# Kernel tuning notes

Measured on AMD Instinct MI355X. Metric: run time of the kernel, lower is better.

## Reference

```python
import math
import jax, jax.numpy as jnp
import numpy as np

B, T, C = 2, 2048, 2048
H, G = 16, 4
D = C // H  # head_dim = 128
KV = G * D
SOFT_CAP = 50.0
EPS = 1e-6


def setup_inputs() -> dict:
    key = jax.random.key(0)
    ks = jax.random.split(key, 5)
    s = 1.0 / math.sqrt(C)
    return {
        "x": jax.random.normal(ks[0], (B, T, C), jnp.float32),
        "Wq": jax.random.normal(ks[1], (C, C), jnp.float32) * s,
        "Wk": jax.random.normal(ks[2], (KV, C), jnp.float32) * s,
        "Wv": jax.random.normal(ks[3], (KV, C), jnp.float32) * s,
        "Wo": jax.random.normal(ks[4], (C, C), jnp.float32) * s,
        "bo": jnp.zeros((C,), jnp.float32),
        "q_norm_w": jnp.ones((D,), jnp.float32),
        "k_norm_w": jnp.ones((D,), jnp.float32),
    }


def _rmsnorm(x, w):
    # norm/sqrt(d) formulation, eps added to rms (matches torch module exactly)
    rms = jnp.linalg.norm(x, axis=-1, keepdims=True) / math.sqrt(x.shape[-1])
    return w * (x / (rms + EPS))


def _rotary_tables(seq_len, dim):
    inv_freq = 1.0 / (10000.0 ** (jnp.arange(0, dim, 2, dtype=jnp.float32) / dim))
    t = jnp.arange(seq_len, dtype=jnp.float32)
    freqs = jnp.outer(t, inv_freq)  # [T, D/2]
    return jnp.cos(freqs), jnp.sin(freqs)


def _apply_rope(x, cos, sin):
    # x: [B, T, h, D]; cos/sin: [T, D/2] broadcast as [1, T, 1, D/2]
    d = x.shape[-1] // 2
    x1, x2 = x[..., :d], x[..., d:]
    c = cos[None, :, None, :]
    s = sin[None, :, None, :]
    return jnp.concatenate([x1 * c + x2 * s, -x1 * s + x2 * c], axis=-1)


def reference(x, Wq, Wk, Wv, Wo, bo, q_norm_w, k_norm_w):
    b, t, c = x.shape
    q = (x @ Wq.T).reshape(b, t, H, D)
    k = (x @ Wk.T).reshape(b, t, G, D)
    v = (x @ Wv.T).reshape(b, t, G, D)

    cos, sin = _rotary_tables(t, D)
    q = _apply_rope(_rmsnorm(q, q_norm_w), cos, sin)
    k = _apply_rope(_rmsnorm(k, k_norm_w), cos, sin)

    q = q.transpose(0, 2, 1, 3)              # [B, H, T, D]
    k = jnp.repeat(k.transpose(0, 2, 1, 3), H // G, axis=1)  # [B, H, T, D]
    v = jnp.repeat(v.transpose(0, 2, 1, 3), H // G, axis=1)

    att = jnp.einsum("bhqd,bhkd->bhqk", q, k) / math.sqrt(D)
    causal = jnp.tril(jnp.ones((t, t), bool))
    att = jnp.where(causal[None, None], att, -jnp.inf)
    att = SOFT_CAP * jnp.tanh(att / SOFT_CAP)  # masked entries -> -50
    att = jax.nn.softmax(att, axis=-1)

    y = jnp.einsum("bhqk,bhkd->bhqd", att, v)
    y = y.transpose(0, 2, 1, 3).reshape(b, t, c)
    return y @ Wo.T + bo
```

## Files before the change

### kernel.cpp

```cpp
#include <hip/hip_runtime.h>
#include <math.h>

#define T_SEQ 2048
#define C_DIM 2048
#define NH    16
#define NG    4
#define DH    128
#define BATCH 2

typedef unsigned short u16;
typedef __bf16 bf16_t;
typedef bf16_t bf16x8 __attribute__((ext_vector_type(8)));
typedef float  f32x4  __attribute__((ext_vector_type(4)));

static __device__ __forceinline__ u16 f2bf(float f) {
    return __builtin_bit_cast(u16, (__bf16)f);
}

static __device__ __forceinline__ void gll16(const void* g, void* lds) {
    __builtin_amdgcn_global_load_lds(
        (const __attribute__((address_space(1))) void*)(unsigned long long)(g),
        (__attribute__((address_space(3))) void*)(unsigned int)(unsigned long long)(lds),
        16, 0, 0);
}

__global__ __launch_bounds__(256)
void cast_multi(const float* __restrict__ x,  const float* __restrict__ wq,
                const float* __restrict__ wk, const float* __restrict__ wv,
                u16* __restrict__ xo, u16* __restrict__ wqo,
                u16* __restrict__ wko, u16* __restrict__ wvo) {
    int i = blockIdx.x * 256 + threadIdx.x;
    const float* src; u16* dst; int off;
    if (i < 1048576)      { src = x;  dst = xo;  off = i; }
    else if (i < 1572864) { src = wq; dst = wqo; off = i - 1048576; }
    else if (i < 1703936) { src = wk; dst = wko; off = i - 1572864; }
    else                  { src = wv; dst = wvo; off = i - 1703936; }
    const float4* p = (const float4*)src + (size_t)off * 2;
    float4 a = p[0], b = p[1];
    u16 u[8] = {f2bf(a.x), f2bf(a.y), f2bf(a.z), f2bf(a.w),
                f2bf(b.x), f2bf(b.y), f2bf(b.z), f2bf(b.w)};
    *(uint4*)(dst + (size_t)off * 8) = *(const uint4*)u;
}

__global__ __launch_bounds__(256)
void cast_f32_bf16(const float* __restrict__ in, u16* __restrict__ out, int n8) {
    int i = blockIdx.x * 256 + threadIdx.x;
    if (i >= n8) return;
    const float4* p = (const float4*)in + (size_t)i * 2;
    float4 a = p[0], b = p[1];
    u16 u[8] = {f2bf(a.x), f2bf(a.y), f2bf(a.z), f2bf(a.w),
                f2bf(b.x), f2bf(b.y), f2bf(b.z), f2bf(b.w)};
    *(uint4*)(out + (size_t)i * 8) = *(const uint4*)u;
}

static __device__ __forceinline__ void gemm_body(
        u16* As, u16* Bs,
        const u16* __restrict__ A, const u16* __restrict__ B,
        const float* __restrict__ bias, float* __restrict__ C,
        int N, int K, int m0, int n0) {
    const int t    = threadIdx.x;
    const int lane = t & 63, w = t >> 6;
    const int l15  = lane & 15, quad = lane >> 4;
    const int wr   = w >> 1, wc = w & 1;

    f32x4 acc[4][4];
#pragma unroll
    for (int mt = 0; mt < 4; ++mt)
#pragma unroll
        for (int nt = 0; nt < 4; ++nt) acc[mt][nt] = (f32x4){0.f, 0.f, 0.f, 0.f};

    const int off0 = w*2048 + lane*16;
    const int r0 = off0 >> 6,          c0 = (off0 & 63) >> 1;
    const int r1 = (off0+1024) >> 6,   c1 = ((off0+1024) & 63) >> 1;
    const u16* Ag0 = A + (size_t)(m0 + r0) * K + c0;
    const u16* Ag1 = A + (size_t)(m0 + r1) * K + c1;
    const u16* Bg0 = B + (size_t)(n0 + r0) * K + c0;
    const u16* Bg1 = B + (size_t)(n0 + r1) * K + c1;
    char* AsB = (char*)As; char* BsB = (char*)Bs;
    const int ldsOff0 = w*2048, ldsOff1 = w*2048 + 1024;

    for (int k0 = 0; k0 < K; k0 += 32) {
        gll16(Ag0 + k0, AsB + ldsOff0);
        gll16(Ag1 + k0, AsB + ldsOff1);
        gll16(Bg0 + k0, BsB + ldsOff0);
        gll16(Bg1 + k0, BsB + ldsOff1);
        __syncthreads();
        bf16x8 af[4], bf[4];
#pragma unroll
        for (int mt = 0; mt < 4; ++mt)
            af[mt] = __builtin_bit_cast(bf16x8,
                *(const uint4*)&As[(wr*64 + mt*16 + l15)*32 + quad*8]);
#pragma unroll
        for (int nt = 0; nt < 4; ++nt)
            bf[nt] = __builtin_bit_cast(bf16x8,
                *(const uint4*)&Bs[(wc*64 + nt*16 + l15)*32 + quad*8]);
#pragma unroll
        for (int mt = 0; mt < 4; ++mt)
#pragma unroll
            for (int nt = 0; nt < 4; ++nt)
                acc[mt][nt] = __builtin_amdgcn_mfma_f32_16x16x32_bf16(
                                  af[mt], bf[nt], acc[mt][nt], 0, 0, 0);
        __syncthreads();
    }

#pragma unroll
    for (int mt = 0; mt < 4; ++mt)
#pragma unroll
        for (int nt = 0; nt < 4; ++nt) {
            const int col = n0 + wc*64 + nt*16 + l15;
            const float bv = bias ? bias[col] : 0.f;
#pragma unroll
            for (int r = 0; r < 4; ++r) {
                const int row = m0 + wr*64 + mt*16 + quad*4 + r;
                C[(size_t)row * N + col] = acc[mt][nt][r] + bv;
            }
        }
}

__global__ __launch_bounds__(256)
void gemm_nt_bf16(const u16* __restrict__ A, const u16* __restrict__ B,
                  const float* __restrict__ bias, float* __restrict__ C,
                  int N, int K) {
    __shared__ __align__(16) u16 As[128*32];
    __shared__ __align__(16) u16 Bs[128*32];
    gemm_body(As, Bs, A, B, bias, C, N, K, blockIdx.y*128, blockIdx.x*128);
}

__global__ __launch_bounds__(256)
void gemm_qkv(const u16* __restrict__ A,  const u16* __restrict__ Bq,
              const u16* __restrict__ Bk, const u16* __restrict__ Bv,
              float* __restrict__ Cq, float* __restrict__ Ck, float* __restrict__ Cv) {
    __shared__ __align__(16) u16 As[128*32];
    __shared__ __align__(16) u16 Bs[128*32];
    const int bx = blockIdx.x;
    const u16* B; float* C; int N, n0;
    if (bx < 16)      { B = Bq; C = Cq; N = 2048; n0 = bx * 128; }
    else if (bx < 20) { B = Bk; C = Ck; N = 512;  n0 = (bx-16) * 128; }
    else              { B = Bv; C = Cv; N = 512;  n0 = (bx-20) * 128; }
    gemm_body(As, Bs, A, B, nullptr, C, N, 2048, blockIdx.y*128, n0);
}

__global__ __launch_bounds__(256)
void rmsnorm_rope_qk(const float* __restrict__ qf, const float* __restrict__ kf,
                     const float* __restrict__ qw, const float* __restrict__ kw,
                     u16* __restrict__ qo, u16* __restrict__ ko) {
    const int blk  = blockIdx.x;
    const int sub  = threadIdx.x >> 6;
    const int lane = threadIdx.x & 63;
    const float* in; const float* w; u16* out; int row, nheads; float scale;
    if (blk < 16384) {
        in = qf; w = qw; out = qo; nheads = NH; scale = 0.08838834764831845f;
        row = blk * 4 + sub;
    } else {
        in = kf; w = kw; out = ko; nheads = NG; scale = 1.0f;
        row = (blk - 16384) * 4 + sub;
    }
    const float* p = in + (size_t)row * 128;
    float x1 = p[lane], x2 = p[lane + 64];
    float ss = x1*x1 + x2*x2;
#pragma unroll
    for (int off = 32; off >= 1; off >>= 1) ss += __shfl_xor(ss, off, 64);
    float inv = 1.0f / (sqrtf(ss * (1.0f/128.0f)) + 1e-6f);
    float x1n = w[lane]      * x1 * inv;
    float x2n = w[lane + 64] * x2 * inv;
    int tpos = (row / nheads) & (T_SEQ - 1);
    float invfreq = powf(10000.0f, -(float)lane / 64.0f);
    float s, c;
    sincosf((float)tpos * invfreq, &s, &c);
    out[(size_t)row*128 + lane]      = f2bf((x1n * c + x2n * s) * scale);
    out[(size_t)row*128 + lane + 64] = f2bf((x2n * c - x1n * s) * scale);
}

__global__ __launch_bounds__(256)
void v_cast_transpose(const float* __restrict__ v, u16* __restrict__ vt) {
    __shared__ u16 Lt[128 * 66];
    const int t  = threadIdx.x;
    const int t0 = blockIdx.x * 64;
    const int bg = blockIdx.y;
    const int b  = bg / NG, g = bg % NG;
#pragma unroll
    for (int rep = 0; rep < 8; ++rep) {
        int idx = rep * 256 + t;
        int i   = idx >> 5;
        int c   = idx & 31;
        float4 f = *(const float4*)(v + ((size_t)(b*T_SEQ + t0 + i)*NG + g)*DH + c*4);
        Lt[(c*4+0)*66 + i] = f2bf(f.x);
        Lt[(c*4+1)*66 + i] = f2bf(f.y);
        Lt[(c*4+2)*66 + i] = f2bf(f.z);
        Lt[(c*4+3)*66 + i] = f2bf(f.w);
    }
    __syncthreads();
#pragma unroll
    for (int rep = 0; rep < 4; ++rep) {
        int idx = rep * 256 + t;
        int d = idx >> 3, c = idx & 7;
        const u16* src = &Lt[d*66 + c*8];
        uint4 val;
        val.x = *(const unsigned int*)(src + 0);
        val.y = *(const unsigned int*)(src + 2);
        val.z = *(const unsigned int*)(src + 4);
        val.w = *(const unsigned int*)(src + 6);
        *(uint4*)(vt + ((size_t)(bg*DH + d))*T_SEQ + t0 + c*8) = val;
    }
}

__global__ __launch_bounds__(256, 2)
void flash_attn_mfma(const u16* __restrict__ qh, const u16* __restrict__ kh,
                     const u16* __restrict__ vt, u16* __restrict__ y) {
    __shared__ __align__(16) u16 Ks[2][64*128];
    __shared__ __align__(16) u16 Vs[2][128*64];
    __shared__ __align__(16) u16 Ps[64*64];

    const int t    = threadIdx.x;
    const int lane = t & 63, w = t >> 6;
    const int l15  = lane & 15, quad = lane >> 4;
    const int bg   = blockIdx.y;
    const int b    = bg >> 2, g = bg & 3;
    const int chunk = b ? (int)blockIdx.x : (63 - (int)blockIdx.x);
    const int q0   = chunk * 32;
    const int h    = g * (NH / NG) + w;

    const float L2E = 1.4426950408889634f;

    bf16x8 aq[2][4];
#pragma unroll
    for (int m = 0; m < 2; ++m) {
        const u16* qp = qh + ((size_t)(b*T_SEQ + q0 + m*16 + l15) * NH + h) * DH;
#pragma unroll
        for (int kc = 0; kc < 4; ++kc)
            aq[m][kc] = __builtin_bit_cast(bf16x8, *(const uint4*)(qp + kc*32 + quad*8));
    }

    f32x4 accO[2][8];
#pragma unroll
    for (int m = 0; m < 2; ++m)
#pragma unroll
        for (int nd = 0; nd < 8; ++nd) accO[m][nd] = (f32x4){0.f, 0.f, 0.f, 0.f};
    float ls[2][4] = {{0.f,0.f,0.f,0.f},{0.f,0.f,0.f,0.f}};

    const u16* kgb = kh + ((size_t)b*T_SEQ*NG + g)*DH;
    const u16* vgb = vt + ((size_t)(b*NG + g)*DH)*T_SEQ;

    const int krb = t >> 4, kcl = t & 15;
    const int vdb = t >> 3, vcl = t & 7;

    const int ktiles = q0/64 + 1;

#pragma unroll
    for (int j = 0; j < 4; ++j) {
        const int kr = j*16 + krb;
        gll16(kgb + (size_t)kr*(NG*DH) + ((kcl ^ (kr & 7)) << 3),
              (char*)Ks[0] + j*4096 + w*1024);
        const int vd = j*32 + vdb;
        gll16(vgb + (size_t)vd*T_SEQ + ((vcl ^ (vd & 7)) << 3),
              (char*)Vs[0] + j*4096 + w*1024);
    }

    for (int kt = 0; kt < ktiles; ++kt) {
        asm volatile("s_waitcnt vmcnt(0)" ::: "memory");
        __syncthreads();

        if (kt + 1 < ktiles) {
            const int k0n = (kt + 1) * 64, bn = (kt + 1) & 1;
#pragma unroll
            for (int j = 0; j < 4; ++j) {
                const int kr = j*16 + krb;
                gll16(kgb + (size_t)(k0n + kr)*(NG*DH) + ((kcl ^ (kr & 7)) << 3),
                      (char*)Ks[bn] + j*4096 + w*1024);
                const int vd = j*32 + vdb;
                gll16(vgb + (size_t)vd*T_SEQ + k0n + ((vcl ^ (vd & 7)) << 3),
                      (char*)Vs[bn] + j*4096 + w*1024);
            }
        }

        const u16* Kb = Ks[kt & 1];
        const u16* Vb = Vs[kt & 1];
        const int k0 = kt * 64;

        f32x4 accS[2][4];
#pragma unroll
        for (int m = 0; m < 2; ++m)
#pragma unroll
            for (int nt = 0; nt < 4; ++nt) accS[m][nt] = (f32x4){0.f,0.f,0.f,0.f};

#pragma unroll
        for (int nt = 0; nt < 4; ++nt) {
            const int krow = nt*16 + l15;
            const int kswz = (krow & 7) << 3;
#pragma unroll
            for (int kc = 0; kc < 4; ++kc) {
                bf16x8 bk = __builtin_bit_cast(bf16x8,
                    *(const uint4*)&Kb[krow*128 + ((kc*32 + quad*8) ^ kswz)]);
                accS[0][nt] = __builtin_amdgcn_mfma_f32_16x16x32_bf16(aq[0][kc], bk, accS[0][nt], 0, 0, 0);
                accS[1][nt] = __builtin_amdgcn_mfma_f32_16x16x32_bf16(aq[1][kc], bk, accS[1][nt], 0, 0, 0);
            }
        }

        bf16x8 ap[2][2];
#pragma unroll
        for (int m = 0; m < 2; ++m) {
#pragma unroll
            for (int nt = 0; nt < 4; ++nt) {
                const int colg = k0 + nt*16 + l15;
#pragma unroll
                for (int r = 0; r < 4; ++r) {
                    const int rowg = q0 + m*16 + quad*4 + r;
                    float s = accS[m][nt][r];
                    float z = s * 0.02f;
                    float u = z * z;
                    float poly = fmaf(u, fmaf(u, fmaf(u, -0.05396825396825397f,
                                           0.13333333333333333f),
                                          -0.3333333333333333f), 1.0f);
                    float p = __builtin_amdgcn_exp2f(s * poly * L2E);
                    p = (colg > rowg) ? 0.f : p;
                    ls[m][r] += p;
                    const int prow = w*16 + quad*4 + r;
                    Ps[prow*64 + ((nt*16 + l15) ^ ((prow & 7) << 3))] = f2bf(p);
                }
            }
            const int arow = w*16 + l15;
            const int aswz = (arow & 7) << 3;
            ap[m][0] = __builtin_bit_cast(bf16x8,
                *(const uint4*)&Ps[arow*64 + ((quad*8)      ^ aswz)]);
            ap[m][1] = __builtin_bit_cast(bf16x8,
                *(const uint4*)&Ps[arow*64 + ((32 + quad*8) ^ aswz)]);
        }

#pragma unroll
        for (int nd = 0; nd < 8; ++nd) {
            const int vrow = nd*16 + l15;
            const int vswz = (vrow & 7) << 3;
#pragma unroll
            for (int kc = 0; kc < 2; ++kc) {
                bf16x8 bv = __builtin_bit_cast(bf16x8,
                    *(const uint4*)&Vb[vrow*64 + ((kc*32 + quad*8) ^ vswz)]);
                accO[0][nd] = __builtin_amdgcn_mfma_f32_16x16x32_bf16(ap[0][kc], bv, accO[0][nd], 0, 0, 0);
                accO[1][nd] = __builtin_amdgcn_mfma_f32_16x16x32_bf16(ap[1][kc], bv, accO[1][nd], 0, 0, 0);
            }
        }
    }

#pragma unroll
    for (int m = 0; m < 2; ++m)
#pragma unroll
        for (int r = 0; r < 4; ++r) {
            float v = ls[m][r];
            v += __shfl_xor(v, 1, 64);
            v += __shfl_xor(v, 2, 64);
            v += __shfl_xor(v, 4, 64);
            v += __shfl_xor(v, 8, 64);
            const float invl = 1.f / v;
            u16* yp = y + (size_t)(b*T_SEQ + q0 + m*16 + quad*4 + r) * C_DIM + h*DH;
#pragma unroll
            for (int nd = 0; nd < 8; ++nd)
                yp[nd*16 + l15] = f2bf(accO[m][nd][r] * invl);
        }
}

extern "C" void kernel_launch(void* const* d_in, const int* in_sizes, int n_in,
                              void* d_out, int out_size, void* d_ws, size_t ws_size,
                              hipStream_t stream) {
    const float* x  = (const float*)d_in[0];
    const float* Wq = (const float*)d_in[1];
    const float* Wk = (const float*)d_in[2];
    const float* Wv = (const float*)d_in[3];
    const float* Wo = (const float*)d_in[4];
    const float* bo = (const float*)d_in[5];
    const float* qw = (const float*)d_in[6];
    const float* kw = (const float*)d_in[7];
    float* out = (float*)d_out;

    const size_t qE = (size_t)BATCH * T_SEQ * NH * DH;
    const size_t kE = (size_t)BATCH * T_SEQ * NG * DH;
    const size_t wqE = (size_t)C_DIM * C_DIM;

    float* qf  = (float*)d_ws;
    float* kf  = qf + qE;
    float* vf  = kf + kE;
    u16*   qh  = (u16*)(vf + kE);
    u16*   khb = qh + qE;
    u16*   vtb = khb + kE;
    u16*   xh  = vtb + kE;
    u16*   wqh = xh + qE;
    u16*   wkh = wqh + wqE;
    u16*   wvh = wkh + (size_t)(NG*DH)*C_DIM;
    u16*   woh = (u16*)kf;
    u16*   yh  = (u16*)qf;

    const int M = BATCH * T_SEQ;
    dim3 blk(256);

    cast_multi<<<dim3(7168), blk, 0, stream>>>(x, Wq, Wk, Wv, xh, wqh, wkh, wvh);

    gemm_qkv<<<dim3(24, M/128), blk, 0, stream>>>(xh, wqh, wkh, wvh, qf, kf, vf);

    rmsnorm_rope_qk<<<dim3(M*NH/4 + M*NG/4), blk, 0, stream>>>(qf, kf, qw, kw, qh, khb);
    v_cast_transpose<<<dim3(T_SEQ/64, BATCH*NG), blk, 0, stream>>>(vf, vtb);

    cast_f32_bf16<<<dim3(wqE/8/256), blk, 0, stream>>>(Wo, woh, wqE/8);

    flash_attn_mfma<<<dim3(T_SEQ/32, BATCH*NG), dim3(256), 0, stream>>>(qh, khb, vtb, yh);

    gemm_nt_bf16<<<dim3(C_DIM/128, M/128), blk, 0, stream>>>(yh, woh, bo, out, C_DIM, C_DIM);
}
```

Baseline: 343.2 us.

## Precompute RoPE tables, restrict causal mask to diagonal tile, add MFMA priority hints

Adds a kernel that precomputes cos/sin RoPE tables once, so the rmsnorm kernel reads them instead of calling powf and sincosf per element. In flash attention, the grid becomes 1D with batch/group interleaved so concurrent blocks share K/V. The causal mask is applied only on the diagonal tile, and the log2(e) factor is folded into the tanh polynomial coefficients. Around the MFMA loops it sets s_setprio, and it changes the P-tile LDS write/read swizzle to reduce bank conflicts. This adds workspace for the tables and an extra launch. The new swizzle indexing must match exactly between the writes and the reads.

New measurement: 343.8 us. Within noise of the previous version (+0.2%).

```diff
diff --git a/kernel.cpp b/kernel.cpp
--- a/kernel.cpp
+++ b/kernel.cpp
@@ -53,6 +53,17 @@
     *(uint4*)(out + (size_t)i * 8) = *(const uint4*)u;
 }
 
+__global__ __launch_bounds__(256)
+void rope_tables(float* __restrict__ cosT, float* __restrict__ sinT) {
+    int i = blockIdx.x * 256 + threadIdx.x;
+    int tp = i >> 6, ln = i & 63;
+    float invfreq = __builtin_amdgcn_exp2f(-(float)ln * (13.287712379549449f / 64.0f));
+    float s, c;
+    sincosf((float)tp * invfreq, &s, &c);
+    cosT[i] = c;
+    sinT[i] = s;
+}
+
 static __device__ __forceinline__ void gemm_body(
         u16* As, u16* Bs,
         const u16* __restrict__ A, const u16* __restrict__ B,
@@ -143,6 +154,7 @@
 __global__ __launch_bounds__(256)
 void rmsnorm_rope_qk(const float* __restrict__ qf, const float* __restrict__ kf,
                      const float* __restrict__ qw, const float* __restrict__ kw,
+                     const float* __restrict__ cosT, const float* __restrict__ sinT,
                      u16* __restrict__ qo, u16* __restrict__ ko) {
     const int blk  = blockIdx.x;
     const int sub  = threadIdx.x >> 6;
@@ -164,9 +176,8 @@
     float x1n = w[lane]      * x1 * inv;
     float x2n = w[lane + 64] * x2 * inv;
     int tpos = (row / nheads) & (T_SEQ - 1);
-    float invfreq = powf(10000.0f, -(float)lane / 64.0f);
-    float s, c;
-    sincosf((float)tpos * invfreq, &s, &c);
+    float c = cosT[tpos*64 + lane];
+    float s = sinT[tpos*64 + lane];
     out[(size_t)row*128 + lane]      = f2bf((x1n * c + x2n * s) * scale);
     out[(size_t)row*128 + lane + 64] = f2bf((x2n * c - x1n * s) * scale);
 }
@@ -214,13 +225,18 @@
     const int t    = threadIdx.x;
     const int lane = t & 63, w = t >> 6;
     const int l15  = lane & 15, quad = lane >> 4;
-    const int bg   = blockIdx.y;
+    const int bid  = blockIdx.x;
+    const int bg   = bid & 7;
     const int b    = bg >> 2, g = bg & 3;
-    const int chunk = b ? (int)blockIdx.x : (63 - (int)blockIdx.x);
+    const int cidx = bid >> 3;
+    const int chunk = b ? cidx : (63 - cidx);
     const int q0   = chunk * 32;
     const int h    = g * (NH / NG) + w;
 
-    const float L2E = 1.4426950408889634f;
+    const float C0 =  1.4426950408889634f;
+    const float C1 = -0.48089834696298777f;
+    const float C2 =  0.19235933878519512f;
+    const float C3 = -0.07785972536301652f;
 
     bf16x8 aq[2][4];
 #pragma unroll
@@ -276,6 +292,7 @@
         const u16* Kb = Ks[kt & 1];
         const u16* Vb = Vs[kt & 1];
         const int k0 = kt * 64;
+        const bool diag = (kt == ktiles - 1);
 
         f32x4 accS[2][4];
 #pragma unroll
@@ -283,6 +300,7 @@
 #pragma unroll
             for (int nt = 0; nt < 4; ++nt) accS[m][nt] = (f32x4){0.f,0.f,0.f,0.f};
 
+        __builtin_amdgcn_s_setprio(1);
 #pragma unroll
         for (int nt = 0; nt < 4; ++nt) {
             const int krow = nt*16 + l15;
@@ -295,6 +313,7 @@
                 accS[1][nt] = __builtin_amdgcn_mfma_f32_16x16x32_bf16(aq[1][kc], bk, accS[1][nt], 0, 0, 0);
             }
         }
+        __builtin_amdgcn_s_setprio(0);
 
         bf16x8 ap[2][2];
 #pragma unroll
@@ -304,28 +323,31 @@
                 const int colg = k0 + nt*16 + l15;
 #pragma unroll
                 for (int r = 0; r < 4; ++r) {
-                    const int rowg = q0 + m*16 + quad*4 + r;
-                    float s = accS[m][nt][r];
-                    float z = s * 0.02f;
+                    float sv = accS[m][nt][r];
+                    float z = sv * 0.02f;
                     float u = z * z;
-                    float poly = fmaf(u, fmaf(u, fmaf(u, -0.05396825396825397f,
-                                           0.13333333333333333f),
-                                          -0.3333333333333333f), 1.0f);
-                    float p = __builtin_amdgcn_exp2f(s * poly * L2E);
-                    p = (colg > rowg) ? 0.f : p;
-                    ls[m][r] += p;
-                    const int prow = w*16 + quad*4 + r;
-                    Ps[prow*64 + ((nt*16 + l15) ^ ((prow & 7) << 3))] = f2bf(p);
+                    float poly = fmaf(u, fmaf(u, fmaf(u, C3, C2), C1), C0);
+                    float pv = __builtin_amdgcn_exp2f(sv * poly);
+                    if (diag) {
+                        const int rowg = q0 + m*16 + quad*4 + r;
+                        pv = (colg > rowg) ? 0.f : pv;
+                    }
+                    ls[m][r] += pv;
+                    const int prow = w*16 + r*4 + quad;
+                    const int pswz = ((quad << 1) | (r & 1)) << 3;
+                    Ps[prow*64 + ((nt*16 + l15) ^ pswz)] = f2bf(pv);
                 }
             }
-            const int arow = w*16 + l15;
-            const int aswz = (arow & 7) << 3;
+            const int srow = (l15 & 3)*4 + (l15 >> 2);
+            const int arow = w*16 + srow;
+            const int aswz = (((l15 >> 2) << 1) | (l15 & 1)) << 3;
             ap[m][0] = __builtin_bit_cast(bf16x8,
                 *(const uint4*)&Ps[arow*64 + ((quad*8)      ^ aswz)]);
             ap[m][1] = __builtin_bit_cast(bf16x8,
                 *(const uint4*)&Ps[arow*64 + ((32 + quad*8) ^ aswz)]);
         }
 
+        __builtin_amdgcn_s_setprio(1);
 #pragma unroll
         for (int nd = 0; nd < 8; ++nd) {
             const int vrow = nd*16 + l15;
@@ -338,6 +360,7 @@
                 accO[1][nd] = __builtin_amdgcn_mfma_f32_16x16x32_bf16(ap[1][kc], bv, accO[1][nd], 0, 0, 0);
             }
         }
+        __builtin_amdgcn_s_setprio(0);
     }
 
 #pragma unroll
@@ -373,6 +396,7 @@
     const size_t qE = (size_t)BATCH * T_SEQ * NH * DH;
     const size_t kE = (size_t)BATCH * T_SEQ * NG * DH;
     const size_t wqE = (size_t)C_DIM * C_DIM;
+    const size_t wkE = (size_t)(NG*DH) * C_DIM;
 
     float* qf  = (float*)d_ws;
     float* kf  = qf + qE;
@@ -383,23 +407,27 @@
     u16*   xh  = vtb + kE;
     u16*   wqh = xh + qE;
     u16*   wkh = wqh + wqE;
-    u16*   wvh = wkh + (size_t)(NG*DH)*C_DIM;
+    u16*   wvh = wkh + wkE;
+    float* cosT = (float*)(wvh + wkE);
+    float* sinT = cosT + 131072;
     u16*   woh = (u16*)kf;
     u16*   yh  = (u16*)qf;
 
     const int M = BATCH * T_SEQ;
     dim3 blk(256);
 
+    rope_tables<<<dim3(512), blk, 0, stream>>>(cosT, sinT);
+
     cast_multi<<<dim3(7168), blk, 0, stream>>>(x, Wq, Wk, Wv, xh, wqh, wkh, wvh);
 
     gemm_qkv<<<dim3(24, M/128), blk, 0, stream>>>(xh, wqh, wkh, wvh, qf, kf, vf);
 
-    rmsnorm_rope_qk<<<dim3(M*NH/4 + M*NG/4), blk, 0, stream>>>(qf, kf, qw, kw, qh, khb);
+    rmsnorm_rope_qk<<<dim3(M*NH/4 + M*NG/4), blk, 0, stream>>>(qf, kf, qw, kw, cosT, sinT, qh, khb);
     v_cast_transpose<<<dim3(T_SEQ/64, BATCH*NG), blk, 0, stream>>>(vf, vtb);
 
     cast_f32_bf16<<<dim3(wqE/8/256), blk, 0, stream>>>(Wo, woh, wqE/8);
 
-    flash_attn_mfma<<<dim3(T_SEQ/32, BATCH*NG), dim3(256), 0, stream>>>(qh, khb, vtb, yh);
+    flash_attn_mfma<<<dim3(512), blk, 0, stream>>>(qh, khb, vtb, yh);
 
     gemm_nt_bf16<<<dim3(C_DIM/128, M/128), blk, 0, stream>>>(yh, woh, bo, out, C_DIM, C_DIM);
 }
```
